# Performance work log

Hardware: AMD Instinct MI355X
Metric: run time of the kernel (lower is better)

Reference implementation:

```python
import jax, jax.numpy as jnp
import numpy as np

B, D, T, R = 8, 128, 32768, 2
C = D // R  # reduced channel dim = 64


def conv1x1(x, w, b):
    # x: [B, Cin, T], w: [Cout, Cin], b: [Cout] -> [B, Cout, T]
    return jnp.einsum('oi,bit->bot', w, x) + b[None, :, None]


def setup_inputs() -> dict:
    key = jax.random.key(0)
    ks = jax.random.split(key, 16)
    inp = {
        'x1': jax.random.normal(ks[0], (B, D, T), dtype=jnp.float32),
        'x2': jnp.zeros((B, D, T), dtype=jnp.float32),  # unused in encoder stage
        'mask': jnp.ones((B, 1, T), dtype=jnp.float32),
        # 1x1 conv projections (weights squeezed to [out, in])
        'wq': jax.random.normal(ks[1], (C, D), dtype=jnp.float32) * 0.05,
        'bq': jnp.zeros((C,), dtype=jnp.float32),
        'wk': jax.random.normal(ks[2], (C, D), dtype=jnp.float32) * 0.05,
        'bk': jnp.zeros((C,), dtype=jnp.float32),
        'wv': jax.random.normal(ks[3], (C, D), dtype=jnp.float32) * 0.05,
        'bv': jnp.zeros((C,), dtype=jnp.float32),
        # E, F: Linear(C -> C) with bias
        'we': jax.random.normal(ks[4], (C, C), dtype=jnp.float32) * 0.1,
        'be': jnp.zeros((C,), dtype=jnp.float32),
        'wf': jax.random.normal(ks[5], (C, C), dtype=jnp.float32) * 0.1,
        'bf': jnp.zeros((C,), dtype=jnp.float32),
        # output 1x1 conv: C -> D
        'wo': jax.random.normal(ks[6], (D, C), dtype=jnp.float32) * 0.05,
        'bo': jnp.zeros((D,), dtype=jnp.float32),
    }
    return inp


def reference(x1, x2, mask, wq, bq, wk, bk, wv, bv, we, be, wf, bf, wo, bo):
    # Q/K/V projections (encoder stage: value from x1; x2 unused)
    Q = conv1x1(x1, wq, bq)              # [B, C, T]
    K = conv1x1(x1, wk, bk)              # [B, C, T]
    V = conv1x1(x1, wv, bv)              # [B, C, T]
    # K = E(K^T): [B, T, C] @ we^T + be
    Kp = jnp.einsum('bct,oc->bto', K, we) + be  # [B, T, C]
    # S = Q @ Kp -> [B, C, C], scaled by sqrt(last dim)
    S = jnp.einsum('bct,btk->bck', Q, Kp)
    P = jax.nn.softmax(S / jnp.sqrt(jnp.asarray(S.shape[-1], S.dtype)), axis=-1)
    # dropout is identity in eval mode
    # V = (F(V^T))^T: [B, C, T]
    Vp = jnp.einsum('bct,oc->bot', V, wf) + bf[None, :, None]  # [B, C, T]
    out = jnp.einsum('bck,bkt->bct', P, Vp)  # [B, C, T]
    out = conv1x1(jax.nn.relu(out), wo, bo)  # [B, D, T]
    return out * mask[:, 0:1, :]
```

## Files before the change

### kernel.cpp

```cpp
#include <hip/hip_runtime.h>
#include <stdint.h>
#include <stddef.h>

#define B_ 8
#define D_ 128
#define T_ 32768
#define C_ 64
#define NCHUNK 32

typedef __bf16 bf16;
typedef __bf16 bf16x8 __attribute__((ext_vector_type(8)));
typedef float f32x4 __attribute__((ext_vector_type(4)));
typedef float f32x16 __attribute__((ext_vector_type(16)));

__device__ __forceinline__ f32x16 zero16() {
  f32x16 z;
#pragma unroll
  for (int i = 0; i < 16; ++i) z[i] = 0.f;
  return z;
}
__device__ __forceinline__ bf16x8 cvt8(f32x4 lo, f32x4 hi) {
  bf16x8 r;
#pragma unroll
  for (int j = 0; j < 4; ++j) { r[j] = (bf16)lo[j]; r[j + 4] = (bf16)hi[j]; }
  return r;
}

__global__ __launch_bounds__(256) void k0_zero(float* __restrict__ p, int n)
{
  int i = blockIdx.x * 256 + threadIdx.x;
  if (i < n) p[i] = 0.f;
}

__global__ __launch_bounds__(256) void k1_gram(
    const float* __restrict__ x1,
    const float* __restrict__ we, const float* __restrict__ wk,
    const float* __restrict__ bk, const float* __restrict__ be,
    const float* __restrict__ wf, const float* __restrict__ wv,
    const float* __restrict__ bv, const float* __restrict__ bfv,
    float* __restrict__ G, float* __restrict__ r,
    float* __restrict__ wkp, float* __restrict__ wvp,
    float* __restrict__ bkp, float* __restrict__ bvp)
{
  const int blk = blockIdx.x;
  const int tid = threadIdx.x;
  const int ngram = B_ * NCHUNK;

  if (blk >= ngram) {
    const int wb = blk - ngram;
    const float* wa  = (wb < 32) ? we : wf;
    const float* wb2 = (wb < 32) ? wk : wv;
    float* outw      = (wb < 32) ? wkp : wvp;
    const int idx = (wb & 31) * 256 + tid;
    const int o = idx >> 7, d = idx & 127;
    float s = 0.f;
    for (int c = 0; c < 64; ++c) s += wa[o * 64 + c] * wb2[c * 128 + d];
    outw[idx] = s;
    if (tid < 64) {
      if (wb == 0) {
        float t = 0.f;
        for (int c = 0; c < 64; ++c) t += we[tid * 64 + c] * bk[c];
        bkp[tid] = t + be[tid];
      } else if (wb == 32) {
        float t = 0.f;
        for (int c = 0; c < 64; ++c) t += wf[tid * 64 + c] * bv[c];
        bvp[tid] = t + bfv[tid];
      }
    }
    return;
  }

  const int b  = blk / NCHUNK;
  const int ch = blk % NCHUNK;
  const int Tc = T_ / NCHUNK;
  const int t0 = ch * Tc;
  const int wave = tid >> 6, lane = tid & 63;
  const int lrow = lane & 31, lk = lane >> 5;
  const int qa = wave >> 1, qb = wave & 1;

  const float* xb = x1 + (size_t)b * D_ * T_;
  const float* pa0 = xb + (size_t)(64 * qa + lrow) * T_ + 8 * lk;
  const float* pa1 = pa0 + (size_t)32 * T_;
  const float* pb0 = xb + (size_t)(64 * qb + lrow) * T_ + 8 * lk;
  const float* pb1 = pb0 + (size_t)32 * T_;

  f32x16 acc00 = zero16(), acc01 = zero16(), acc10 = zero16(), acc11 = zero16();
  float rsum = 0.f;

  for (int t = t0; t < t0 + Tc; t += 16) {
    f32x4 a0l = *(const f32x4*)(pa0 + t), a0h = *(const f32x4*)(pa0 + t + 4);
    f32x4 a1l = *(const f32x4*)(pa1 + t), a1h = *(const f32x4*)(pa1 + t + 4);
    f32x4 b0l = *(const f32x4*)(pb0 + t), b0h = *(const f32x4*)(pb0 + t + 4);
    f32x4 b1l = *(const f32x4*)(pb1 + t), b1h = *(const f32x4*)(pb1 + t + 4);
    bf16x8 fa0 = cvt8(a0l, a0h);
    bf16x8 fa1 = cvt8(a1l, a1h);
    bf16x8 fb0 = cvt8(b0l, b0h);
    bf16x8 fb1 = cvt8(b1l, b1h);
    f32x4 ol = qb ? a1l : a0l, oh = qb ? a1h : a0h;
#pragma unroll
    for (int j = 0; j < 4; ++j) rsum += ol[j] + oh[j];
    acc00 = __builtin_amdgcn_mfma_f32_32x32x16_bf16(fa0, fb0, acc00, 0, 0, 0);
    acc01 = __builtin_amdgcn_mfma_f32_32x32x16_bf16(fa0, fb1, acc01, 0, 0, 0);
    acc10 = __builtin_amdgcn_mfma_f32_32x32x16_bf16(fa1, fb0, acc10, 0, 0, 0);
    acc11 = __builtin_amdgcn_mfma_f32_32x32x16_bf16(fa1, fb1, acc11, 0, 0, 0);
  }

  float* gb = G + (size_t)b * 16384;
#pragma unroll
  for (int rr = 0; rr < 16; ++rr) {
    const int rloc = (rr & 3) + 8 * (rr >> 2) + 4 * lk;
    const int r0 = 64 * qa + rloc, r1 = 64 * qa + 32 + rloc;
    const int c0 = 64 * qb + lrow, c1 = 64 * qb + 32 + lrow;
    atomicAdd(&gb[r0 * 128 + c0], acc00[rr]);
    atomicAdd(&gb[r0 * 128 + c1], acc01[rr]);
    atomicAdd(&gb[r1 * 128 + c0], acc10[rr]);
    atomicAdd(&gb[r1 * 128 + c1], acc11[rr]);
  }
  float rtot = rsum + __shfl_xor(rsum, 32, 64);
  if (lk == 0) atomicAdd(&r[b * 128 + 32 * wave + lrow], rtot);
}

__global__ __launch_bounds__(128) void k3_softmax(
    const float* __restrict__ wq, const float* __restrict__ bq,
    const float* __restrict__ G, const float* __restrict__ r,
    const float* __restrict__ wkp, const float* __restrict__ wvp,
    const float* __restrict__ bkp, const float* __restrict__ bvp,
    bf16* __restrict__ attw, float* __restrict__ attb)
{
  const int b = blockIdx.x >> 6, c = blockIdx.x & 63;
  const int tid = threadIdx.x;
  __shared__ float sM[128], sR[128], sQ[128], sP[64];
  __shared__ float sRed;

  const float* Gb = G + (size_t)b * 16384;
  const float* wqc = wq + c * 128;

  const float rv = r[b * 128 + tid];
  sR[tid] = rv;
  float m = 0.f;
  for (int j = 0; j < 128; ++j) m += wqc[j] * Gb[j * 128 + tid];
  sM[tid] = m;
  sQ[tid] = wqc[tid] * rv;
  __syncthreads();

  if (tid < 64) {
    float q2 = sQ[tid] + sQ[tid + 64];
#pragma unroll
    for (int off = 32; off; off >>= 1) q2 += __shfl_xor(q2, off, 64);
    if (tid == 0) sRed = q2;
  }
  __syncthreads();
  const float qr = sRed;
  const float bqc = bq[c];

  if (tid < 64) {
    const int k = tid;
    float s = 0.f, wkr = 0.f;
    for (int i = 0; i < 128; ++i) {
      const float w = wkp[k * 128 + i];
      s += sM[i] * w;
      wkr += sR[i] * w;
    }
    const float bk2 = bkp[k];
    float logit = (s + bqc * wkr + bk2 * qr + (float)T_ * bqc * bk2) * 0.125f;
    float mx = logit;
#pragma unroll
    for (int off = 32; off; off >>= 1) mx = fmaxf(mx, __shfl_xor(mx, off, 64));
    const float e = __expf(logit - mx);
    float sum = e;
#pragma unroll
    for (int off = 32; off; off >>= 1) sum += __shfl_xor(sum, off, 64);
    sP[k] = e / sum;
  }
  __syncthreads();

  {
    float aw = 0.f;
    for (int k = 0; k < 64; ++k) aw += sP[k] * wvp[k * 128 + tid];
    attw[((size_t)b * 64 + c) * 128 + tid] = (bf16)aw;
  }
  if (tid < 64) {
    float pb = sP[tid] * bvp[tid];
#pragma unroll
    for (int off = 32; off; off >>= 1) pb += __shfl_xor(pb, off, 64);
    if (tid == 0) attb[b * 64 + c] = pb;
  }
}

__global__ __launch_bounds__(256) void k4_out(
    const float* __restrict__ x1, const float* __restrict__ mask,
    const float* __restrict__ wo, const float* __restrict__ bo,
    const bf16* __restrict__ attw, const float* __restrict__ attb,
    float* __restrict__ out)
{
  __shared__ bf16 x_lds[128 * 128];
  __shared__ bf16 m1_lds[64 * 128];
  __shared__ float bo_lds[128];
  __shared__ float ab_lds[64];

  const int b = blockIdx.x >> 8;
  const int t0 = (blockIdx.x & 255) * 128;
  const int tid = threadIdx.x;
  const int wave = tid >> 6, lane = tid & 63;
  const int lrow = lane & 31, lk = lane >> 5;
  const float* xb = x1 + (size_t)b * D_ * T_;

  {
    const int dr = tid >> 4;
    const int tc = (tid & 15) * 8;
#pragma unroll
    for (int it = 0; it < 8; ++it) {
      const int d = it * 16 + dr;
      f32x4 lo = *(const f32x4*)(xb + (size_t)d * T_ + t0 + tc);
      f32x4 hi = *(const f32x4*)(xb + (size_t)d * T_ + t0 + tc + 4);
      *(bf16x8*)&x_lds[d * 128 + tc] = cvt8(lo, hi);
    }
  }
  if (tid < 128) bo_lds[tid] = bo[tid];
  if (tid < 64) ab_lds[tid] = attb[b * 64 + tid];
  __syncthreads();

  const int tcol = 32 * wave + lrow;

  f32x16 p0 = zero16(), p1 = zero16();
  const bf16* awb = attw + (size_t)b * 64 * 128;
#pragma unroll
  for (int k0 = 0; k0 < 128; k0 += 16) {
    bf16x8 a0 = *(const bf16x8*)(awb + (size_t)(lrow) * 128 + k0 + 8 * lk);
    bf16x8 a1 = *(const bf16x8*)(awb + (size_t)(32 + lrow) * 128 + k0 + 8 * lk);
    bf16x8 bx;
#pragma unroll
    for (int j = 0; j < 8; ++j) bx[j] = x_lds[(k0 + 8 * lk + j) * 128 + tcol];
    p0 = __builtin_amdgcn_mfma_f32_32x32x16_bf16(a0, bx, p0, 0, 0, 0);
    p1 = __builtin_amdgcn_mfma_f32_32x32x16_bf16(a1, bx, p1, 0, 0, 0);
  }
#pragma unroll
  for (int rr = 0; rr < 16; ++rr) {
    const int row = (rr & 3) + 8 * (rr >> 2) + 4 * lk;
    m1_lds[row * 128 + tcol]        = (bf16)fmaxf(p0[rr] + ab_lds[row], 0.f);
    m1_lds[(32 + row) * 128 + tcol] = (bf16)fmaxf(p1[rr] + ab_lds[32 + row], 0.f);
  }
  __syncthreads();

  f32x16 q0 = zero16(), q1 = zero16(), q2 = zero16(), q3 = zero16();
#pragma unroll
  for (int k0 = 0; k0 < 64; k0 += 16) {
    bf16x8 bm;
#pragma unroll
    for (int j = 0; j < 8; ++j) bm[j] = m1_lds[(k0 + 8 * lk + j) * 128 + tcol];
#pragma unroll
    for (int i = 0; i < 4; ++i) {
      const float* wrow = wo + (size_t)(32 * i + lrow) * 64 + k0 + 8 * lk;
      bf16x8 wfrag = cvt8(*(const f32x4*)wrow, *(const f32x4*)(wrow + 4));
      if (i == 0) q0 = __builtin_amdgcn_mfma_f32_32x32x16_bf16(wfrag, bm, q0, 0, 0, 0);
      if (i == 1) q1 = __builtin_amdgcn_mfma_f32_32x32x16_bf16(wfrag, bm, q1, 0, 0, 0);
      if (i == 2) q2 = __builtin_amdgcn_mfma_f32_32x32x16_bf16(wfrag, bm, q2, 0, 0, 0);
      if (i == 3) q3 = __builtin_amdgcn_mfma_f32_32x32x16_bf16(wfrag, bm, q3, 0, 0, 0);
    }
  }

  const float mv = mask[(size_t)b * T_ + t0 + tcol];
  float* ob = out + (size_t)b * D_ * T_ + t0 + tcol;
#pragma unroll
  for (int rr = 0; rr < 16; ++rr) {
    const int row = (rr & 3) + 8 * (rr >> 2) + 4 * lk;
    ob[(size_t)(row) * T_]      = (q0[rr] + bo_lds[row]) * mv;
    ob[(size_t)(32 + row) * T_] = (q1[rr] + bo_lds[32 + row]) * mv;
    ob[(size_t)(64 + row) * T_] = (q2[rr] + bo_lds[64 + row]) * mv;
    ob[(size_t)(96 + row) * T_] = (q3[rr] + bo_lds[96 + row]) * mv;
  }
}

extern "C" void kernel_launch(void* const* d_in, const int* in_sizes, int n_in,
                              void* d_out, int out_size, void* d_ws, size_t ws_size,
                              hipStream_t stream)
{
  const float* x1   = (const float*)d_in[0];
  const float* mask = (const float*)d_in[2];
  const float* wq   = (const float*)d_in[3];
  const float* bq   = (const float*)d_in[4];
  const float* wk   = (const float*)d_in[5];
  const float* bk   = (const float*)d_in[6];
  const float* wv   = (const float*)d_in[7];
  const float* bv   = (const float*)d_in[8];
  const float* we   = (const float*)d_in[9];
  const float* be   = (const float*)d_in[10];
  const float* wf   = (const float*)d_in[11];
  const float* bfv  = (const float*)d_in[12];
  const float* wo   = (const float*)d_in[13];
  const float* bo   = (const float*)d_in[14];
  float* out = (float*)d_out;

  float* G   = (float*)d_ws;
  float* r   = G + (size_t)B_ * 16384;
  float* wkp = r + B_ * 128;
  float* wvp = wkp + 8192;
  float* bkp = wvp + 8192;
  float* bvp = bkp + 64;
  float* attb = bvp + 64;
  bf16*  attw = (bf16*)(attb + B_ * 64);

  const int nzero = B_ * 16384 + B_ * 128;
  k0_zero<<<(nzero + 255) / 256, 256, 0, stream>>>(G, nzero);
  k1_gram<<<B_ * NCHUNK + 64, 256, 0, stream>>>(x1, we, wk, bk, be, wf, wv, bv, bfv,
                                                G, r, wkp, wvp, bkp, bvp);
  k3_softmax<<<B_ * 64, 128, 0, stream>>>(wq, bq, G, r, wkp, wvp, bkp, bvp, attw, attb);
  k4_out<<<B_ * (T_ / 128), 256, 0, stream>>>(x1, mask, wo, bo, attw, attb, out);
}
```

Measured before the change: 425.1 us.

## Cache bf16 copy of x in workspace and replace gram atomics with partial reduce

The gram kernel now also writes a bf16 copy of x1, which the output kernel loads directly into LDS via global_load_lds instead of reloading and converting fp32 data. When workspace allows, per-chunk gram partials are written and summed in a new reduce kernel instead of using atomics and a zero kernel. The output kernel aliases its intermediate buffer into the x tile to cut LDS and raise occupancy. This adds extra write traffic for the bf16 copy and the partials, and the path chosen depends on workspace size.

```diff
diff --git a/kernel.cpp b/kernel.cpp
--- a/kernel.cpp
+++ b/kernel.cpp
@@ -6,7 +6,6 @@
 #define D_ 128
 #define T_ 32768
 #define C_ 64
-#define NCHUNK 32
 
 typedef __bf16 bf16;
 typedef __bf16 bf16x8 __attribute__((ext_vector_type(8)));
@@ -24,6 +23,11 @@
 #pragma unroll
   for (int j = 0; j < 4; ++j) { r[j] = (bf16)lo[j]; r[j + 4] = (bf16)hi[j]; }
   return r;
+}
+__device__ __forceinline__ void load_lds16(const bf16* g, bf16* l) {
+  __builtin_amdgcn_global_load_lds(
+      (const __attribute__((address_space(1))) void*)g,
+      (__attribute__((address_space(3))) void*)l, 16, 0, 0);
 }
 
 __global__ __launch_bounds__(256) void k0_zero(float* __restrict__ p, int n)
@@ -39,12 +43,15 @@
     const float* __restrict__ wf, const float* __restrict__ wv,
     const float* __restrict__ bv, const float* __restrict__ bfv,
     float* __restrict__ G, float* __restrict__ r,
+    float* __restrict__ Gp, float* __restrict__ rp,
     float* __restrict__ wkp, float* __restrict__ wvp,
-    float* __restrict__ bkp, float* __restrict__ bvp)
+    float* __restrict__ bkp, float* __restrict__ bvp,
+    bf16* __restrict__ xbf,
+    int nchunk, int use_atomic, int use_xbf)
 {
   const int blk = blockIdx.x;
   const int tid = threadIdx.x;
-  const int ngram = B_ * NCHUNK;
+  const int ngram = B_ * nchunk;
 
   if (blk >= ngram) {
     const int wb = blk - ngram;
@@ -70,9 +77,9 @@
     return;
   }
 
-  const int b  = blk / NCHUNK;
-  const int ch = blk % NCHUNK;
-  const int Tc = T_ / NCHUNK;
+  const int b  = blk / nchunk;
+  const int ch = blk % nchunk;
+  const int Tc = T_ / nchunk;
   const int t0 = ch * Tc;
   const int wave = tid >> 6, lane = tid & 63;
   const int lrow = lane & 31, lk = lane >> 5;
@@ -83,6 +90,8 @@
   const float* pa1 = pa0 + (size_t)32 * T_;
   const float* pb0 = xb + (size_t)(64 * qb + lrow) * T_ + 8 * lk;
   const float* pb1 = pb0 + (size_t)32 * T_;
+  bf16* xo = use_xbf ? (xbf + (size_t)b * D_ * T_ + (size_t)(64 * qa + lrow) * T_ + 8 * lk)
+                     : (bf16*)nullptr;
 
   f32x16 acc00 = zero16(), acc01 = zero16(), acc10 = zero16(), acc11 = zero16();
   float rsum = 0.f;
@@ -96,6 +105,10 @@
     bf16x8 fa1 = cvt8(a1l, a1h);
     bf16x8 fb0 = cvt8(b0l, b0h);
     bf16x8 fb1 = cvt8(b1l, b1h);
+    if (use_xbf && qb == 0) {
+      *(bf16x8*)(xo + t) = fa0;
+      *(bf16x8*)(xo + (size_t)32 * T_ + t) = fa1;
+    }
     f32x4 ol = qb ? a1l : a0l, oh = qb ? a1h : a0h;
 #pragma unroll
     for (int j = 0; j < 4; ++j) rsum += ol[j] + oh[j];
@@ -105,19 +118,57 @@
     acc11 = __builtin_amdgcn_mfma_f32_32x32x16_bf16(fa1, fb1, acc11, 0, 0, 0);
   }
 
-  float* gb = G + (size_t)b * 16384;
-#pragma unroll
-  for (int rr = 0; rr < 16; ++rr) {
-    const int rloc = (rr & 3) + 8 * (rr >> 2) + 4 * lk;
-    const int r0 = 64 * qa + rloc, r1 = 64 * qa + 32 + rloc;
-    const int c0 = 64 * qb + lrow, c1 = 64 * qb + 32 + lrow;
-    atomicAdd(&gb[r0 * 128 + c0], acc00[rr]);
-    atomicAdd(&gb[r0 * 128 + c1], acc01[rr]);
-    atomicAdd(&gb[r1 * 128 + c0], acc10[rr]);
-    atomicAdd(&gb[r1 * 128 + c1], acc11[rr]);
-  }
   float rtot = rsum + __shfl_xor(rsum, 32, 64);
-  if (lk == 0) atomicAdd(&r[b * 128 + 32 * wave + lrow], rtot);
+
+  if (use_atomic) {
+    float* gb = G + (size_t)b * 16384;
+#pragma unroll
+    for (int rr = 0; rr < 16; ++rr) {
+      const int rloc = (rr & 3) + 8 * (rr >> 2) + 4 * lk;
+      const int r0 = 64 * qa + rloc, r1 = 64 * qa + 32 + rloc;
+      const int c0 = 64 * qb + lrow, c1 = 64 * qb + 32 + lrow;
+      atomicAdd(&gb[r0 * 128 + c0], acc00[rr]);
+      atomicAdd(&gb[r0 * 128 + c1], acc01[rr]);
+      atomicAdd(&gb[r1 * 128 + c0], acc10[rr]);
+      atomicAdd(&gb[r1 * 128 + c1], acc11[rr]);
+    }
+    if (lk == 0) atomicAdd(&r[b * 128 + 32 * wave + lrow], rtot);
+  } else {
+    float* gb = Gp + (size_t)(b * nchunk + ch) * 16384;
+#pragma unroll
+    for (int rr = 0; rr < 16; ++rr) {
+      const int rloc = (rr & 3) + 8 * (rr >> 2) + 4 * lk;
+      const int r0 = 64 * qa + rloc, r1 = 64 * qa + 32 + rloc;
+      const int c0 = 64 * qb + lrow, c1 = 64 * qb + 32 + lrow;
+      gb[r0 * 128 + c0] = acc00[rr];
+      gb[r0 * 128 + c1] = acc01[rr];
+      gb[r1 * 128 + c0] = acc10[rr];
+      gb[r1 * 128 + c1] = acc11[rr];
+    }
+    if (lk == 0) rp[(size_t)(b * nchunk + ch) * 128 + 32 * wave + lrow] = rtot;
+  }
+}
+
+__global__ __launch_bounds__(256) void k2_reduce(
+    const float* __restrict__ Gp, const float* __restrict__ rp,
+    float* __restrict__ G, float* __restrict__ r, int nchunk)
+{
+  const int b = blockIdx.x >> 4, part = blockIdx.x & 15;
+  const int tid = threadIdx.x;
+  const float* gpb = Gp + (size_t)b * nchunk * 16384;
+#pragma unroll
+  for (int q = 0; q < 4; ++q) {
+    const int idx = part * 1024 + q * 256 + tid;
+    float s = 0.f;
+    for (int ch = 0; ch < nchunk; ++ch) s += gpb[(size_t)ch * 16384 + idx];
+    G[(size_t)b * 16384 + idx] = s;
+  }
+  if (part == 0 && tid < 128) {
+    const float* rpb = rp + (size_t)b * nchunk * 128;
+    float s = 0.f;
+    for (int ch = 0; ch < nchunk; ++ch) s += rpb[ch * 128 + tid];
+    r[b * 128 + tid] = s;
+  }
 }
 
 __global__ __launch_bounds__(128) void k3_softmax(
@@ -187,25 +238,34 @@
   }
 }
 
-__global__ __launch_bounds__(256) void k4_out(
-    const float* __restrict__ x1, const float* __restrict__ mask,
+__global__ __launch_bounds__(256, 4) void k4_out(
+    const float* __restrict__ x1, const bf16* __restrict__ xbf,
+    const float* __restrict__ mask,
     const float* __restrict__ wo, const float* __restrict__ bo,
     const bf16* __restrict__ attw, const float* __restrict__ attb,
-    float* __restrict__ out)
+    float* __restrict__ out, int use_xbf)
 {
   __shared__ bf16 x_lds[128 * 128];
-  __shared__ bf16 m1_lds[64 * 128];
   __shared__ float bo_lds[128];
   __shared__ float ab_lds[64];
+  bf16* m1_lds = &x_lds[64 * 128];
 
   const int b = blockIdx.x >> 8;
   const int t0 = (blockIdx.x & 255) * 128;
   const int tid = threadIdx.x;
   const int wave = tid >> 6, lane = tid & 63;
   const int lrow = lane & 31, lk = lane >> 5;
-  const float* xb = x1 + (size_t)b * D_ * T_;
-
-  {
+
+  if (use_xbf) {
+    const bf16* xbb = xbf + (size_t)b * D_ * T_ + t0;
+#pragma unroll
+    for (int i = 0; i < 8; ++i) {
+      const int d0 = 32 * wave + 4 * i;
+      const bf16* src = xbb + (size_t)(d0 + (lane >> 4)) * T_ + (lane & 15) * 8;
+      load_lds16(src, &x_lds[d0 * 128]);
+    }
+  } else {
+    const float* xb = x1 + (size_t)b * D_ * T_;
     const int dr = tid >> 4;
     const int tc = (tid & 15) * 8;
 #pragma unroll
@@ -240,7 +300,6 @@
     m1_lds[row * 128 + tcol]        = (bf16)fmaxf(p0[rr] + ab_lds[row], 0.f);
     m1_lds[(32 + row) * 128 + tcol] = (bf16)fmaxf(p1[rr] + ab_lds[32 + row], 0.f);
   }
-  __syncthreads();
 
   f32x16 q0 = zero16(), q1 = zero16(), q2 = zero16(), q3 = zero16();
 #pragma unroll
@@ -291,19 +350,49 @@
   const float* bo   = (const float*)d_in[14];
   float* out = (float*)d_out;
 
-  float* G   = (float*)d_ws;
-  float* r   = G + (size_t)B_ * 16384;
-  float* wkp = r + B_ * 128;
-  float* wvp = wkp + 8192;
-  float* bkp = wvp + 8192;
-  float* bvp = bkp + 64;
-  float* attb = bvp + 64;
-  bf16*  attw = (bf16*)(attb + B_ * 64);
-
-  const int nzero = B_ * 16384 + B_ * 128;
-  k0_zero<<<(nzero + 255) / 256, 256, 0, stream>>>(G, nzero);
-  k1_gram<<<B_ * NCHUNK + 64, 256, 0, stream>>>(x1, we, wk, bk, be, wf, wv, bv, bfv,
-                                                G, r, wkp, wvp, bkp, bvp);
+  char* base = (char*)d_ws;
+  size_t off = 0;
+  float* G   = (float*)(base + off); off += (size_t)B_ * 16384 * 4;
+  float* r   = (float*)(base + off); off += (size_t)B_ * 128 * 4;
+  float* wkp = (float*)(base + off); off += 8192 * 4;
+  float* wvp = (float*)(base + off); off += 8192 * 4;
+  float* bkp = (float*)(base + off); off += 64 * 4;
+  float* bvp = (float*)(base + off); off += 64 * 4;
+  float* attb = (float*)(base + off); off += (size_t)B_ * 64 * 4;
+  bf16* attw = (bf16*)(base + off); off += (size_t)B_ * 64 * 128 * 2;
+  off = (off + 255) & ~(size_t)255;
+  const size_t fixed_end = off;
+
+  const size_t xbf_bytes = (size_t)B_ * D_ * T_ * 2;
+  auto gp_bytes = [](int nc) {
+    return (size_t)B_ * nc * 16384 * 4 + (size_t)B_ * nc * 128 * 4;
+  };
+
+  int nchunk, use_atomic, use_xbf;
+  size_t gp_off;
+  if (ws_size >= fixed_end + xbf_bytes + gp_bytes(64)) {
+    use_xbf = 1; use_atomic = 0; nchunk = 64; gp_off = fixed_end + xbf_bytes;
+  } else if (ws_size >= fixed_end + xbf_bytes) {
+    use_xbf = 1; use_atomic = 1; nchunk = 32; gp_off = fixed_end;
+  } else if (ws_size >= fixed_end + gp_bytes(32)) {
+    use_xbf = 0; use_atomic = 0; nchunk = 32; gp_off = fixed_end;
+  } else {
+    use_xbf = 0; use_atomic = 1; nchunk = 32; gp_off = fixed_end;
+  }
+  bf16* xbf = (bf16*)(base + fixed_end);
+  float* Gp = (float*)(base + gp_off);
+  float* rp = Gp + (size_t)B_ * nchunk * 16384;
+
+  if (use_atomic) {
+    const int nzero = B_ * 16384 + B_ * 128;
+    k0_zero<<<(nzero + 255) / 256, 256, 0, stream>>>(G, nzero);
+  }
+  k1_gram<<<B_ * nchunk + 64, 256, 0, stream>>>(
+      x1, we, wk, bk, be, wf, wv, bv, bfv,
+      G, r, Gp, rp, wkp, wvp, bkp, bvp, xbf, nchunk, use_atomic, use_xbf);
+  if (!use_atomic)
+    k2_reduce<<<B_ * 16, 256, 0, stream>>>(Gp, rp, G, r, nchunk);
   k3_softmax<<<B_ * 64, 128, 0, stream>>>(wq, bq, G, r, wkp, wvp, bkp, bvp, attw, attb);
-  k4_out<<<B_ * (T_ / 128), 256, 0, stream>>>(x1, mask, wo, bo, attw, attb, out);
-}
+  k4_out<<<B_ * (T_ / 128), 256, 0, stream>>>(x1, xbf, mask, wo, bo, attw, attb, out,
+                                              use_xbf);
+}
```

After: 528.1 us. +24.2%, slower.
